# Kernel tuning notes

Measured on AMD Instinct MI355X. Metric: run time of the kernel, lower is better.

The kernel has to match this reference:

```python
import jax, jax.numpy as jnp
import numpy as np

N_EMBED = 1024
SEQ_LEN = 2048
BATCH = 4


def setup_inputs() -> dict:
    key = jax.random.key(0)
    ks = jax.random.split(key, 9)
    E = N_EMBED
    x = jax.random.normal(ks[0], (BATCH, SEQ_LEN, E), dtype=jnp.float32)
    s = 0.02
    return {
        "x": x,
        "Wq": jax.random.normal(ks[1], (E, E), dtype=jnp.float32) * s,
        "bq": jnp.zeros((E,), dtype=jnp.float32),
        "Wk": jax.random.normal(ks[2], (E, E), dtype=jnp.float32) * s,
        "bk": jnp.zeros((E,), dtype=jnp.float32),
        "Wv": jax.random.normal(ks[3], (E, E), dtype=jnp.float32) * s,
        "bv": jnp.zeros((E,), dtype=jnp.float32),
        "Wp": jax.random.normal(ks[4], (E, E), dtype=jnp.float32) * s,
        "bp": jnp.zeros((E,), dtype=jnp.float32),
    }


def reference(x, Wq, bq, Wk, bk, Wv, bv, Wp, bp):
    # x: [B, S, E]. Original torch code unpacks (B, C, N) = x.shape and
    # scales by sqrt(C) == sqrt(seq_len)  (a bug we faithfully replicate).
    B, S, E = x.shape
    q = jnp.einsum('bse,fe->bsf', x, Wq) + bq
    k = jnp.einsum('bse,fe->bsf', x, Wk) + bk
    v = jnp.einsum('bse,fe->bsf', x, Wv) + bv
    scale = 1.0 / jnp.sqrt(jnp.asarray(S, dtype=x.dtype))
    scores = jnp.einsum('bqe,bke->bqk', q, k) * scale  # [B, S, S]
    # NOTE: original calls masked_fill (non-inplace) and discards the result,
    # so NO causal mask is actually applied. Replicate that: plain softmax.
    w = jax.nn.softmax(scores, axis=-1)
    o = jnp.einsum('bqk,bke->bqe', w, v)
    out = jnp.einsum('bse,fe->bsf', o, Wp) + bp
    return out
```

## Files before the change

### kernel.cpp

```cpp
#include <hip/hip_runtime.h>


typedef __bf16 bf16x8 __attribute__((ext_vector_type(8)));
typedef float  f32x4  __attribute__((ext_vector_type(4)));
typedef unsigned short u16x8 __attribute__((ext_vector_type(8)));

__device__ __forceinline__ float bf2f(unsigned short u) {
  return __uint_as_float(((unsigned int)u) << 16);
}
__device__ __forceinline__ unsigned short f2bf(float f) {
  unsigned int u = __float_as_uint(f);
  return (unsigned short)((u + 0x7fffu + ((u >> 16) & 1u)) >> 16);
}
__device__ __forceinline__ void gload16(const void* g, void* l) {
  __builtin_amdgcn_global_load_lds(
      (const __attribute__((address_space(1))) void*)g,
      (__attribute__((address_space(3))) void*)l, 16, 0, 0);
}

__global__ __launch_bounds__(256) void cvt_all(
    const float* __restrict__ x, const float* __restrict__ wq,
    const float* __restrict__ wk, const float* __restrict__ wv,
    const float* __restrict__ wp, unsigned short* __restrict__ x_bf,
    unsigned short* __restrict__ wc, unsigned short* __restrict__ wpb) {
  const float* s;
  unsigned short* d;
  int i;
  if (blockIdx.x < 4096) {
    s = x; d = x_bf;
    i = (blockIdx.x * 256 + threadIdx.x) * 8;
  } else {
    const int b = blockIdx.x - 4096;
    const int seg = b >> 9;
    i = ((b & 511) * 256 + threadIdx.x) * 8;
    if (seg == 0)      { s = wq; d = wc; }
    else if (seg == 1) { s = wk; d = wc + 1048576; }
    else if (seg == 2) { s = wv; d = wc + 2097152; }
    else               { s = wp; d = wpb; }
  }
  f32x4 a = *(const f32x4*)(s + i);
  f32x4 b = *(const f32x4*)(s + i + 4);
  u16x8 o;
  o[0] = f2bf(a[0]); o[1] = f2bf(a[1]); o[2] = f2bf(a[2]); o[3] = f2bf(a[3]);
  o[4] = f2bf(b[0]); o[5] = f2bf(b[1]); o[6] = f2bf(b[2]); o[7] = f2bf(b[3]);
  *(u16x8*)(d + i) = o;
}

template <int EPI>
__device__ __forceinline__ void gemm_core(
    const unsigned short* __restrict__ A, const unsigned short* __restrict__ B,
    void* __restrict__ C0, void* __restrict__ C1, void* __restrict__ C2,
    const float* __restrict__ bias0, const float* __restrict__ bias1,
    const float* __restrict__ bias2, const float* __restrict__ rowsum,
    int K, long long sA, long long sB, long long sC,
    int nbm, int nbn, int ldc, float scale) {
  __shared__ char lds[147456];
  char* ldsA = lds;
  char* ldsB = lds + 98304;

  const int nwg = (int)gridDim.x;
  int id = (int)blockIdx.x;
  id = (id & 7) * (nwg >> 3) + (id >> 3);
  const int nbmn = nbm * nbn;
  const int bz = id / nbmn;
  const int rem = id - bz * nbmn;
  const int bm = rem / nbn;
  const int bn = rem - bm * nbn;
  const int gm0 = bm * 256, gn0 = bn * 128;

  const unsigned short* Ag = A + (size_t)bz * sA;
  const unsigned short* Bg = B + (size_t)bz * sB;

  const int tid = threadIdx.x;
  const int w = tid >> 6, l = tid & 63;
  const int wr = w >> 1, wc = w & 1;
  const int lr = l & 15;
  const int lk16 = (l >> 4) * 16;
  const int swz = (lr & 7) << 4;

  const int srow = tid >> 3;
  const int sbo  = ((tid & 7) * 16) ^ ((srow & 7) << 4);
  const int sdst = tid * 16;

#define STG_A(region, ktile)                                                   \
  do {                                                                         \
    const char* _b = (const char*)(Ag + (size_t)(gm0 + srow) * K) +            \
                     (size_t)(ktile) * 128 + sbo;                              \
    const size_t _rk = (size_t)64 * K * 2;                                     \
    gload16(_b,           (region) + sdst);                                    \
    gload16(_b + _rk,     (region) + 8192 + sdst);                             \
    gload16(_b + 2 * _rk, (region) + 16384 + sdst);                            \
    gload16(_b + 3 * _rk, (region) + 24576 + sdst);                            \
  } while (0)
#define STG_B(region, ktile)                                                   \
  do {                                                                         \
    const char* _b = (const char*)(Bg + (size_t)(gn0 + srow) * K) +            \
                     (size_t)(ktile) * 128 + sbo;                              \
    const size_t _rk = (size_t)64 * K * 2;                                     \
    gload16(_b,       (region) + sdst);                                        \
    gload16(_b + _rk, (region) + 8192 + sdst);                                 \
  } while (0)

#define RD_A(dst, m, kh)                                                       \
  dst = *(const bf16x8*)(Abuf + (wr * 64 + (m) * 16 + lr) * 128 +              \
                         ((lk16 + (kh) * 64) ^ swz))
#define RD_B(dst, n, kh)                                                       \
  dst = *(const bf16x8*)(Bbuf + (wc * 64 + (n) * 16 + lr) * 128 +              \
                         ((lk16 + (kh) * 64) ^ swz))

#define LGKM_PIN()                                          \
  asm volatile("s_waitcnt lgkmcnt(0)" ::: "memory");        \
  __builtin_amdgcn_sched_barrier(0)

  f32x4 acc[4][4];
#pragma unroll
  for (int i = 0; i < 4; ++i)
#pragma unroll
    for (int j = 0; j < 4; ++j) acc[i][j] = (f32x4){0.f, 0.f, 0.f, 0.f};

  const int nt = K >> 6;

  STG_B(ldsB, 0); STG_A(ldsA, 0);
  if (nt > 1) { STG_B(ldsB + 16384, 1); STG_A(ldsA + 32768, 1); }
  if (nt > 1) { asm volatile("s_waitcnt vmcnt(6)" ::: "memory"); }
  else        { asm volatile("s_waitcnt vmcnt(0)" ::: "memory"); }
  __builtin_amdgcn_s_barrier();

  int cur = 0;
  for (int t = 0; t < nt; ++t) {
    char* Abuf = ldsA + cur * 32768;
    char* Bbuf = ldsB + cur * 16384;
    const int nx2 = (cur + 2 >= 3) ? cur - 1 : cur + 2;
    const bool pf = (t + 2 < nt);

    bf16x8 af[4], bfr[4];
#pragma unroll
    for (int m = 0; m < 4; ++m) RD_A(af[m], m, 0);
#pragma unroll
    for (int n = 0; n < 4; ++n) RD_B(bfr[n], n, 0);
    if (pf) STG_B(ldsB + nx2 * 16384, t + 2);
    __builtin_amdgcn_s_barrier();
    LGKM_PIN();
    __builtin_amdgcn_s_setprio(1);
#pragma unroll
    for (int m = 0; m < 4; ++m)
#pragma unroll
      for (int n = 0; n < 4; ++n)
        acc[m][n] = __builtin_amdgcn_mfma_f32_16x16x32_bf16(af[m], bfr[n],
                                                            acc[m][n], 0, 0, 0);
    __builtin_amdgcn_s_setprio(0);
    __builtin_amdgcn_s_barrier();

#pragma unroll
    for (int m = 0; m < 4; ++m) RD_A(af[m], m, 1);
#pragma unroll
    for (int n = 0; n < 4; ++n) RD_B(bfr[n], n, 1);
    if (pf) STG_A(ldsA + nx2 * 32768, t + 2);
    __builtin_amdgcn_s_barrier();
    LGKM_PIN();
    __builtin_amdgcn_s_setprio(1);
#pragma unroll
    for (int m = 0; m < 4; ++m)
#pragma unroll
      for (int n = 0; n < 4; ++n)
        acc[m][n] = __builtin_amdgcn_mfma_f32_16x16x32_bf16(af[m], bfr[n],
                                                            acc[m][n], 0, 0, 0);
    __builtin_amdgcn_s_setprio(0);
    if (pf)              { asm volatile("s_waitcnt vmcnt(6)" ::: "memory"); }
    else if (t + 1 < nt) { asm volatile("s_waitcnt vmcnt(0)" ::: "memory"); }
    __builtin_amdgcn_s_barrier();

    cur = (cur + 1 >= 3) ? 0 : cur + 1;
  }

  const int cr = (l >> 4) * 4;
  const int cc = l & 15;
#pragma unroll
  for (int m = 0; m < 4; ++m) {
    const int row = gm0 + wr * 64 + m * 16 + cr;
    if constexpr (EPI == 3) {
      const float* rs = rowsum + bz * 2048 + row;
      const f32x4 rv = *(const f32x4*)rs;
      f32x4 inv;
#pragma unroll
      for (int j = 0; j < 4; ++j) inv[j] = 1.0f / rv[j];
      float* Cp = (float*)C0 + (size_t)bz * sC;
#pragma unroll
      for (int n = 0; n < 4; ++n) {
        const int col = gn0 + wc * 64 + n * 16 + cc;
        const float b = bias0[col];
        f32x4 a = acc[m][n];
#pragma unroll
        for (int j = 0; j < 4; ++j)
          Cp[(size_t)(row + j) * ldc + col] = a[j] * inv[j] + b;
      }
    } else {
#pragma unroll
      for (int n = 0; n < 4; ++n) {
        const int col = gn0 + wc * 64 + n * 16 + cc;
        f32x4 a = acc[m][n];
        if constexpr (EPI == 0) {
          const int g = gn0 >> 10;
          const int cl = col & 1023;
          unsigned short* Cp;
          float b;
          if (g == 0)      { Cp = (unsigned short*)C0; b = bias0[cl]; }
          else if (g == 1) { Cp = (unsigned short*)C1; b = bias1[cl]; }
          else             { Cp = (unsigned short*)C2; b = bias2[cl]; }
          if (g == 0) {
#pragma unroll
            for (int j = 0; j < 4; ++j)
              Cp[(size_t)(row + j) * 1024 + cl] = f2bf((a[j] + b) * scale);
          } else {
#pragma unroll
            for (int j = 0; j < 4; ++j)
              Cp[(size_t)(row + j) * 1024 + cl] = f2bf(a[j] + b);
          }
        } else {
          unsigned short* Cp = (unsigned short*)C0 + (size_t)bz * sC;
#pragma unroll
          for (int j = 0; j < 4; ++j)
            Cp[(size_t)(row + j) * ldc + col] = f2bf(a[j]);
        }
      }
    }
  }
#undef STG_A
#undef STG_B
#undef RD_A
#undef RD_B
#undef LGKM_PIN
}

__global__ __launch_bounds__(512) void gqkv(
    const unsigned short* A, const unsigned short* B, void* Q, void* Kd,
    void* V, const float* bq, const float* bk, const float* bv, float scale) {
  gemm_core<0>(A, B, Q, Kd, V, bq, bk, bv, nullptr,
               1024, 0, 0, 0, 32, 24, 1024, scale);
}
__global__ __launch_bounds__(512) void gvwt(
    const unsigned short* A, const unsigned short* B, void* C) {
  gemm_core<1>(A, B, C, nullptr, nullptr, nullptr, nullptr, nullptr, nullptr,
               1024, 0, 2097152, 2097152, 4, 16, 2048, 0.f);
}
__global__ __launch_bounds__(512) void gout(
    const unsigned short* A, const unsigned short* B, void* C,
    const float* bp, const float* rowsum) {
  gemm_core<3>(A, B, C, nullptr, nullptr, bp, nullptr, nullptr,
               rowsum, 2048, 4194304, 2097152, 2097152, 8, 8, 1024, 0.f);
}

__global__ __launch_bounds__(512) void gsco8(
    const unsigned short* __restrict__ A, const unsigned short* __restrict__ B,
    unsigned short* __restrict__ C, float* __restrict__ rowsum,
    int K, long long sA, long long sB, long long sC, int nbm, int nbn) {
  __shared__ char lds[131072];
  char* ldsA = lds;
  char* ldsB = lds + 65536;

  const int nwg = (int)gridDim.x;
  int id = (int)blockIdx.x;
  id = (id & 7) * (nwg >> 3) + (id >> 3);
  const int nbmn = nbm * nbn;
  const int bz = id / nbmn;
  const int rem = id - bz * nbmn;
  const int bm = rem / nbn;
  const int bn = rem - bm * nbn;
  const int gm0 = bm * 256, gn0 = bn * 256;

  const unsigned short* Ag = A + (size_t)bz * sA;
  const unsigned short* Bg = B + (size_t)bz * sB;

  const int tid = threadIdx.x;
  const int w = tid >> 6, l = tid & 63;
  const int wr = w >> 2, wc = w & 3;
  const int lr = l & 15;
  const int lk16 = (l >> 4) * 16;
  const int swz = (lr & 7) << 4;

  const int srow0 = (tid * 16) >> 7;
  const int srow1 = srow0 + 64;
  const int sbo   = ((tid * 16) & 127) ^ ((srow0 & 7) << 4);
  const int sdst0 = tid * 16;
  const int sdst1 = tid * 16 + 8192;

#define STAGE(gbase, grow0, region, ktile)                                     \
  do {                                                                         \
    const char* _s0 =                                                          \
        (const char*)((gbase) + (size_t)((grow0) + srow0) * K) +               \
        (ktile) * 128 + sbo;                                                   \
    const char* _s1 =                                                          \
        (const char*)((gbase) + (size_t)((grow0) + srow1) * K) +               \
        (ktile) * 128 + sbo;                                                   \
    gload16(_s0, (region) + sdst0);                                            \
    gload16(_s1, (region) + sdst1);                                            \
  } while (0)

#define RDA(dst, m, kh) \
  dst = *(const bf16x8*)(Areg + ((m) * 16 + lr) * 128 + ((lk16 + (kh) * 64) ^ swz))
#define RDB(dst, n, kh) \
  dst = *(const bf16x8*)(Breg + (((wc & 1) * 64 + (n) * 16 + lr) * 128) + ((lk16 + (kh) * 64) ^ swz))

  f32x4 acc[8][4];
#pragma unroll
  for (int i = 0; i < 8; ++i)
#pragma unroll
    for (int j = 0; j < 4; ++j) acc[i][j] = (f32x4){0.f, 0.f, 0.f, 0.f};

  bf16x8 af[4][2], bf_[4][2];

#define MM(mi, ai, n)                                                          \
  acc[mi][n] = __builtin_amdgcn_mfma_f32_16x16x32_bf16(af[ai][0], bf_[n][0],   \
                                                       acc[mi][n], 0, 0, 0);   \
  acc[mi][n] = __builtin_amdgcn_mfma_f32_16x16x32_bf16(af[ai][1], bf_[n][1],   \
                                                       acc[mi][n], 0, 0, 0)

#define LGKM_PIN()                                          \
  asm volatile("s_waitcnt lgkmcnt(0)" ::: "memory");        \
  __builtin_amdgcn_sched_barrier(0)

  const int nt = K >> 6;

  STAGE(Bg, gn0,       ldsB + 0,     0);
  STAGE(Bg, gn0 + 128, ldsB + 16384, 0);
  STAGE(Ag, gm0,       ldsA + 0,     0);
  STAGE(Ag, gm0 + 128, ldsA + 16384, 0);
  STAGE(Bg, gn0,       ldsB + 32768,         1);
  STAGE(Bg, gn0 + 128, ldsB + 32768 + 16384, 1);
  STAGE(Ag, gm0,       ldsA + 32768,         1);
  asm volatile("s_waitcnt vmcnt(6)" ::: "memory");
  __builtin_amdgcn_s_barrier();

  for (int t = 0; t < nt; ++t) {
    const int cur = t & 1;
    char* Areg  = ldsA + cur * 32768 + wr * 16384;
    char* Breg  = ldsB + cur * 32768 + (wc >> 1) * 16384;
    char* Anext = ldsA + (cur ^ 1) * 32768;
    char* Acur2 = ldsA + cur * 32768;
    char* Bcur2 = ldsB + cur * 32768;

#pragma unroll
    for (int m = 0; m < 4; ++m) { RDA(af[m][0], m, 0); RDA(af[m][1], m, 1); }
#pragma unroll
    for (int n = 0; n < 2; ++n) { RDB(bf_[n][0], n, 0); RDB(bf_[n][1], n, 1); }
    if (wc < 2) {
#pragma unroll
      for (int n = 2; n < 4; ++n) { RDB(bf_[n][0], n, 0); RDB(bf_[n][1], n, 1); }
    }
    if (t + 1 < nt) STAGE(Ag, gm0 + 128, Anext + 16384, t + 1);
    __builtin_amdgcn_s_barrier();
    LGKM_PIN();
    __builtin_amdgcn_s_setprio(1);
    MM(0, 0, 0); MM(0, 0, 1); MM(1, 1, 0); MM(1, 1, 1);
    MM(2, 2, 0); MM(2, 2, 1); MM(3, 3, 0); MM(3, 3, 1);
    __builtin_amdgcn_s_setprio(0);
    __builtin_amdgcn_s_barrier();

    if (wc >= 2) {
#pragma unroll
      for (int n = 2; n < 4; ++n) { RDB(bf_[n][0], n, 0); RDB(bf_[n][1], n, 1); }
    }
    if (t + 2 < nt) STAGE(Bg, gn0, Bcur2, t + 2);
    __builtin_amdgcn_s_barrier();
    LGKM_PIN();
    __builtin_amdgcn_s_setprio(1);
    MM(0, 0, 2); MM(0, 0, 3); MM(1, 1, 2); MM(1, 1, 3);
    MM(2, 2, 2); MM(2, 2, 3); MM(3, 3, 2); MM(3, 3, 3);
    __builtin_amdgcn_s_setprio(0);
    __builtin_amdgcn_s_barrier();

#pragma unroll
    for (int m = 0; m < 4; ++m) { RDA(af[m][0], m + 4, 0); RDA(af[m][1], m + 4, 1); }
    if (t + 2 < nt) STAGE(Bg, gn0 + 128, Bcur2 + 16384, t + 2);
    __builtin_amdgcn_s_barrier();
    LGKM_PIN();
    __builtin_amdgcn_s_setprio(1);
    MM(4, 0, 0); MM(4, 0, 1); MM(5, 1, 0); MM(5, 1, 1);
    MM(6, 2, 0); MM(6, 2, 1); MM(7, 3, 0); MM(7, 3, 1);
    __builtin_amdgcn_s_setprio(0);
    __builtin_amdgcn_s_barrier();

    if (t + 2 < nt) STAGE(Ag, gm0, Acur2, t + 2);
    __builtin_amdgcn_s_barrier();
    __builtin_amdgcn_s_setprio(1);
    MM(4, 0, 2); MM(4, 0, 3); MM(5, 1, 2); MM(5, 1, 3);
    MM(6, 2, 2); MM(6, 2, 3); MM(7, 3, 2); MM(7, 3, 3);
    __builtin_amdgcn_s_setprio(0);
    if (t + 2 < nt) {
      asm volatile("s_waitcnt vmcnt(6)" ::: "memory");
    } else {
      asm volatile("s_waitcnt vmcnt(0)" ::: "memory");
    }
    __builtin_amdgcn_s_barrier();
  }

  const int cr = (l >> 4) * 4;
  const int cc = l & 15;
  unsigned short* Cp = C + (size_t)bz * sC;
#pragma unroll
  for (int m = 0; m < 8; ++m) {
    const int row = gm0 + wr * 128 + m * 16 + cr;
    float psum[4] = {0.f, 0.f, 0.f, 0.f};
#pragma unroll
    for (int n = 0; n < 4; ++n) {
      const int col = gn0 + wc * 64 + n * 16 + cc;
      f32x4 a = acc[m][n];
#pragma unroll
      for (int j = 0; j < 4; ++j) {
        const unsigned short us = f2bf(__expf(a[j]));
        Cp[(size_t)(row + j) * 2048 + col] = us;
        psum[j] += bf2f(us);
      }
    }
#pragma unroll
    for (int j = 0; j < 4; ++j) {
#pragma unroll
      for (int i = 1; i < 16; i <<= 1) psum[j] += __shfl_xor(psum[j], i, 16);
      if ((l & 15) == 0) atomicAdd(rowsum + bz * 2048 + row + j, psum[j]);
    }
  }
#undef STAGE
#undef RDA
#undef RDB
#undef MM
#undef LGKM_PIN
}

extern "C" void kernel_launch(void* const* d_in, const int* in_sizes, int n_in,
                              void* d_out, int out_size, void* d_ws, size_t ws_size,
                              hipStream_t stream) {
  const float* x  = (const float*)d_in[0];
  const float* Wq = (const float*)d_in[1];
  const float* bq = (const float*)d_in[2];
  const float* Wk = (const float*)d_in[3];
  const float* bk = (const float*)d_in[4];
  const float* Wv = (const float*)d_in[5];
  const float* bv = (const float*)d_in[6];
  const float* Wp = (const float*)d_in[7];
  const float* bp = (const float*)d_in[8];
  float* out = (float*)d_out;

  char* ws = (char*)d_ws;
  unsigned short* x_bf  = (unsigned short*)(ws);
  unsigned short* Wc    = (unsigned short*)(ws + (16ull << 20));
  unsigned short* Wp_bf = (unsigned short*)(ws + (22ull << 20));
  unsigned short* Qm    = (unsigned short*)(ws + (24ull << 20));
  unsigned short* Km    = (unsigned short*)(ws + (40ull << 20));
  unsigned short* Vm    = (unsigned short*)(ws + (56ull << 20));
  unsigned short* VWt   = (unsigned short*)(ws + (72ull << 20));
  unsigned short* Em    = (unsigned short*)(ws + (88ull << 20));
  float* rowsum = (float*)(ws + (56ull << 20));

  const float scale = 0.022097086912079608f;

  cvt_all<<<6144, 256, 0, stream>>>(x, Wq, Wk, Wv, Wp, x_bf, Wc, Wp_bf);

  gqkv<<<768, 512, 0, stream>>>(x_bf, Wc, Qm, Km, Vm, bq, bk, bv, scale);
  gvwt<<<256, 512, 0, stream>>>(Wp_bf, Vm, VWt);
  (void)hipMemsetAsync(rowsum, 0, 8192 * sizeof(float), stream);
  gsco8<<<256, 512, 0, stream>>>(Qm, Km, Em, rowsum,
                                 1024, 2097152, 2097152, 4194304, 8, 8);
  gout<<<256, 512, 0, stream>>>(Em, VWt, out, bp, rowsum);
}
```

Measured before the change: 184.7 us.

## Fold Q/K/V projections into precomputed weight products to skip per-token projections

```diff
diff --git a/kernel.cpp b/kernel.cpp
--- a/kernel.cpp
+++ b/kernel.cpp
@@ -18,25 +18,16 @@
       (__attribute__((address_space(3))) void*)l, 16, 0, 0);
 }
 
-__global__ __launch_bounds__(256) void cvt_all(
-    const float* __restrict__ x, const float* __restrict__ wq,
-    const float* __restrict__ wk, const float* __restrict__ wv,
-    const float* __restrict__ wp, unsigned short* __restrict__ x_bf,
-    unsigned short* __restrict__ wc, unsigned short* __restrict__ wpb) {
+__global__ __launch_bounds__(256) void cvt_str(
+    const float* __restrict__ x, const float* __restrict__ wp,
+    unsigned short* __restrict__ x_bf, unsigned short* __restrict__ wp_bf) {
   const float* s;
   unsigned short* d;
   int i;
   if (blockIdx.x < 4096) {
-    s = x; d = x_bf;
-    i = (blockIdx.x * 256 + threadIdx.x) * 8;
+    s = x; d = x_bf; i = (blockIdx.x * 256 + threadIdx.x) * 8;
   } else {
-    const int b = blockIdx.x - 4096;
-    const int seg = b >> 9;
-    i = ((b & 511) * 256 + threadIdx.x) * 8;
-    if (seg == 0)      { s = wq; d = wc; }
-    else if (seg == 1) { s = wk; d = wc + 1048576; }
-    else if (seg == 2) { s = wv; d = wc + 2097152; }
-    else               { s = wp; d = wpb; }
+    s = wp; d = wp_bf; i = ((blockIdx.x - 4096) * 256 + threadIdx.x) * 8;
   }
   f32x4 a = *(const f32x4*)(s + i);
   f32x4 b = *(const f32x4*)(s + i + 4);
@@ -46,20 +37,78 @@
   *(u16x8*)(d + i) = o;
 }
 
+__global__ __launch_bounds__(256) void cvt_T(
+    const float* __restrict__ wq, const float* __restrict__ wk,
+    const float* __restrict__ wv, unsigned short* __restrict__ qt,
+    unsigned short* __restrict__ kt, unsigned short* __restrict__ vt) {
+  const float* in;
+  unsigned short* out;
+  int b = blockIdx.x;
+  if (b < 256)      { in = wq; out = qt; }
+  else if (b < 512) { in = wk; out = kt; b -= 256; }
+  else              { in = wv; out = vt; b -= 512; }
+  const int r0 = (b >> 4) * 64, c0 = (b & 15) * 64;
+  __shared__ unsigned short t[64][72];
+  const int tid = threadIdx.x;
+  const int rr = tid >> 4;
+  const int cc4 = (tid & 15) * 4;
+#pragma unroll
+  for (int p = 0; p < 4; ++p) {
+    const int r = rr + p * 16;
+    f32x4 v = *(const f32x4*)(in + (size_t)(r0 + r) * 1024 + c0 + cc4);
+    t[cc4 + 0][r] = f2bf(v[0]);
+    t[cc4 + 1][r] = f2bf(v[1]);
+    t[cc4 + 2][r] = f2bf(v[2]);
+    t[cc4 + 3][r] = f2bf(v[3]);
+  }
+  __syncthreads();
+  const int wr_ = tid >> 3;
+  const int wc8 = (tid & 7) * 8;
+#pragma unroll
+  for (int p = 0; p < 2; ++p) {
+    const int c = wr_ + p * 32;
+    u16x8 o;
+#pragma unroll
+    for (int j = 0; j < 8; ++j) o[j] = t[c][wc8 + j];
+    *(u16x8*)(out + (size_t)(c0 + c) * 1024 + r0 + wc8) = o;
+  }
+}
+
+__global__ __launch_bounds__(256) void cvec(
+    const float* __restrict__ bq, const float* __restrict__ Wk,
+    const float* __restrict__ Wp, const float* __restrict__ bv,
+    float* __restrict__ c1, float* __restrict__ cv, float scale) {
+  if (blockIdx.x < 4) {
+    const int e = blockIdx.x * 256 + threadIdx.x;
+    float acc = 0.f;
+    for (int f = 0; f < 1024; ++f) acc += bq[f] * Wk[(size_t)f * 1024 + e];
+    c1[e] = acc * scale;
+  } else {
+    const int e = blockIdx.x - 4;
+    float acc = 0.f;
+    for (int f = threadIdx.x; f < 1024; f += 256)
+      acc += Wp[(size_t)e * 1024 + f] * bv[f];
+#pragma unroll
+    for (int i = 1; i < 64; i <<= 1) acc += __shfl_xor(acc, i, 64);
+    __shared__ float red[4];
+    if ((threadIdx.x & 63) == 0) red[threadIdx.x >> 6] = acc;
+    __syncthreads();
+    if (threadIdx.x == 0) cv[e] = red[0] + red[1] + red[2] + red[3];
+  }
+}
+
 template <int EPI>
 __device__ __forceinline__ void gemm_core(
+    char* lds, int nwg, int base,
     const unsigned short* __restrict__ A, const unsigned short* __restrict__ B,
-    void* __restrict__ C0, void* __restrict__ C1, void* __restrict__ C2,
-    const float* __restrict__ bias0, const float* __restrict__ bias1,
-    const float* __restrict__ bias2, const float* __restrict__ rowsum,
+    void* __restrict__ C, const float* __restrict__ bias,
+    const float* __restrict__ rowsum,
     int K, long long sA, long long sB, long long sC,
     int nbm, int nbn, int ldc, float scale) {
-  __shared__ char lds[147456];
   char* ldsA = lds;
   char* ldsB = lds + 98304;
 
-  const int nwg = (int)gridDim.x;
-  int id = (int)blockIdx.x;
+  int id = (int)blockIdx.x - base;
   id = (id & 7) * (nwg >> 3) + (id >> 3);
   const int nbmn = nbm * nbn;
   const int bz = id / nbmn;
@@ -184,43 +233,29 @@
       f32x4 inv;
 #pragma unroll
       for (int j = 0; j < 4; ++j) inv[j] = 1.0f / rv[j];
-      float* Cp = (float*)C0 + (size_t)bz * sC;
+      float* Cp = (float*)C + (size_t)bz * sC;
 #pragma unroll
       for (int n = 0; n < 4; ++n) {
         const int col = gn0 + wc * 64 + n * 16 + cc;
-        const float b = bias0[col];
+        const float b = bias[col];
         f32x4 a = acc[m][n];
 #pragma unroll
         for (int j = 0; j < 4; ++j)
           Cp[(size_t)(row + j) * ldc + col] = a[j] * inv[j] + b;
       }
     } else {
+      unsigned short* Cp = (unsigned short*)C + (size_t)bz * sC;
 #pragma unroll
       for (int n = 0; n < 4; ++n) {
         const int col = gn0 + wc * 64 + n * 16 + cc;
         f32x4 a = acc[m][n];
-        if constexpr (EPI == 0) {
-          const int g = gn0 >> 10;
-          const int cl = col & 1023;
-          unsigned short* Cp;
-          float b;
-          if (g == 0)      { Cp = (unsigned short*)C0; b = bias0[cl]; }
-          else if (g == 1) { Cp = (unsigned short*)C1; b = bias1[cl]; }
-          else             { Cp = (unsigned short*)C2; b = bias2[cl]; }
-          if (g == 0) {
-#pragma unroll
-            for (int j = 0; j < 4; ++j)
-              Cp[(size_t)(row + j) * 1024 + cl] = f2bf((a[j] + b) * scale);
-          } else {
-#pragma unroll
-            for (int j = 0; j < 4; ++j)
-              Cp[(size_t)(row + j) * 1024 + cl] = f2bf(a[j] + b);
-          }
-        } else {
-          unsigned short* Cp = (unsigned short*)C0 + (size_t)bz * sC;
-#pragma unroll
-          for (int j = 0; j < 4; ++j)
-            Cp[(size_t)(row + j) * ldc + col] = f2bf(a[j]);
+#pragma unroll
+        for (int j = 0; j < 4; ++j) {
+          float v;
+          if constexpr (EPI == 1)      v = a[j] * scale;
+          else if constexpr (EPI == 4) v = a[j] + bias[row + j];
+          else                         v = a[j] + bias[col];
+          Cp[(size_t)(row + j) * ldc + col] = f2bf(v);
         }
       }
     }
@@ -232,22 +267,38 @@
 #undef LGKM_PIN
 }
 
-__global__ __launch_bounds__(512) void gqkv(
-    const unsigned short* A, const unsigned short* B, void* Q, void* Kd,
-    void* V, const float* bq, const float* bk, const float* bv, float scale) {
-  gemm_core<0>(A, B, Q, Kd, V, bq, bk, bv, nullptr,
-               1024, 0, 0, 0, 32, 24, 1024, scale);
+__global__ __launch_bounds__(512) void gweights(
+    const unsigned short* WkT, const unsigned short* WqT,
+    const unsigned short* Wp, const unsigned short* WvT,
+    unsigned short* HT, unsigned short* G, float scale) {
+  __shared__ char lds[147456];
+  if (blockIdx.x < 32)
+    gemm_core<1>(lds, 32, 0, WkT, WqT, HT, nullptr, nullptr,
+                 1024, 0, 0, 0, 4, 8, 1024, scale);
+  else
+    gemm_core<1>(lds, 32, 32, Wp, WvT, G, nullptr, nullptr,
+                 1024, 0, 0, 0, 4, 8, 1024, 1.0f);
+}
+__global__ __launch_bounds__(512) void gr(
+    const unsigned short* x, const unsigned short* HT, unsigned short* R,
+    const float* c1) {
+  __shared__ char lds[147456];
+  gemm_core<5>(lds, 256, 0, x, HT, R, c1, nullptr,
+               1024, 0, 0, 0, 32, 8, 1024, 0.f);
 }
 __global__ __launch_bounds__(512) void gvwt(
-    const unsigned short* A, const unsigned short* B, void* C) {
-  gemm_core<1>(A, B, C, nullptr, nullptr, nullptr, nullptr, nullptr, nullptr,
+    const unsigned short* G, const unsigned short* x, unsigned short* VWt,
+    const float* cv) {
+  __shared__ char lds[147456];
+  gemm_core<4>(lds, 256, 0, G, x, VWt, cv, nullptr,
                1024, 0, 2097152, 2097152, 4, 16, 2048, 0.f);
 }
 __global__ __launch_bounds__(512) void gout(
-    const unsigned short* A, const unsigned short* B, void* C,
+    const unsigned short* E, const unsigned short* VWt, float* out,
     const float* bp, const float* rowsum) {
-  gemm_core<3>(A, B, C, nullptr, nullptr, bp, nullptr, nullptr,
-               rowsum, 2048, 4194304, 2097152, 2097152, 8, 8, 1024, 0.f);
+  __shared__ char lds[147456];
+  gemm_core<3>(lds, 256, 0, E, VWt, out, bp, rowsum,
+               2048, 4194304, 2097152, 2097152, 8, 8, 1024, 0.f);
 }
 
 __global__ __launch_bounds__(512) void gsco8(
@@ -433,7 +484,7 @@
   const float* Wq = (const float*)d_in[1];
   const float* bq = (const float*)d_in[2];
   const float* Wk = (const float*)d_in[3];
-  const float* bk = (const float*)d_in[4];
+  const float* bk = (const float*)d_in[4];  (void)bk;
   const float* Wv = (const float*)d_in[5];
   const float* bv = (const float*)d_in[6];
   const float* Wp = (const float*)d_in[7];
@@ -442,23 +493,29 @@
 
   char* ws = (char*)d_ws;
   unsigned short* x_bf  = (unsigned short*)(ws);
-  unsigned short* Wc    = (unsigned short*)(ws + (16ull << 20));
-  unsigned short* Wp_bf = (unsigned short*)(ws + (22ull << 20));
-  unsigned short* Qm    = (unsigned short*)(ws + (24ull << 20));
-  unsigned short* Km    = (unsigned short*)(ws + (40ull << 20));
-  unsigned short* Vm    = (unsigned short*)(ws + (56ull << 20));
-  unsigned short* VWt   = (unsigned short*)(ws + (72ull << 20));
-  unsigned short* Em    = (unsigned short*)(ws + (88ull << 20));
-  float* rowsum = (float*)(ws + (56ull << 20));
+  unsigned short* Wp_bf = (unsigned short*)(ws + (16ull << 20));
+  unsigned short* WqT   = (unsigned short*)(ws + (18ull << 20));
+  unsigned short* WkT   = (unsigned short*)(ws + (20ull << 20));
+  unsigned short* WvT   = (unsigned short*)(ws + (22ull << 20));
+  unsigned short* HT    = (unsigned short*)(ws + (24ull << 20));
+  unsigned short* G     = (unsigned short*)(ws + (26ull << 20));
+  float*          c1    = (float*)(ws + (28ull << 20));
+  float*          cv    = (float*)(ws + (28ull << 20) + 65536);
+  unsigned short* R     = (unsigned short*)(ws + (32ull << 20));
+  unsigned short* VWt   = (unsigned short*)(ws + (48ull << 20));
+  unsigned short* Em    = (unsigned short*)(ws + (64ull << 20));
+  float*          rowsum = (float*)(ws + (96ull << 20));
 
   const float scale = 0.022097086912079608f;
 
-  cvt_all<<<6144, 256, 0, stream>>>(x, Wq, Wk, Wv, Wp, x_bf, Wc, Wp_bf);
-
-  gqkv<<<768, 512, 0, stream>>>(x_bf, Wc, Qm, Km, Vm, bq, bk, bv, scale);
-  gvwt<<<256, 512, 0, stream>>>(Wp_bf, Vm, VWt);
+  cvt_str<<<4608, 256, 0, stream>>>(x, Wp, x_bf, Wp_bf);
+  cvt_T<<<768, 256, 0, stream>>>(Wq, Wk, Wv, WqT, WkT, WvT);
+  cvec<<<1028, 256, 0, stream>>>(bq, Wk, Wp, bv, c1, cv, scale);
+  gweights<<<64, 512, 0, stream>>>(WkT, WqT, Wp_bf, WvT, HT, G, scale);
+  gr<<<256, 512, 0, stream>>>(x_bf, HT, R, c1);
+  gvwt<<<256, 512, 0, stream>>>(G, x_bf, VWt, cv);
   (void)hipMemsetAsync(rowsum, 0, 8192 * sizeof(float), stream);
-  gsco8<<<256, 512, 0, stream>>>(Qm, Km, Em, rowsum,
+  gsco8<<<256, 512, 0, stream>>>(R, x_bf, Em, rowsum,
                                  1024, 2097152, 2097152, 4194304, 8, 8);
   gout<<<256, 512, 0, stream>>>(Em, VWt, out, bp, rowsum);
 }
```

Result: slower. 188.7 us (+2.2%).
